# Performance work log

Measured on AMD Instinct MI355X. Metric: run time of the kernel, lower is better.

The kernel has to match this reference:

```python
import jax, jax.numpy as jnp
import numpy as np

B, C, H, W = 8, 512, 64, 64
WS, NH = 8, 16
HD = C // NH
SCALE = float(HD) ** -0.5
L = WS * WS  # tokens per window
BN_EPS = 1e-5


def _rel_index():
    # Swin relative position index, (L, L) int table into (2*WS-1)^2 bias rows
    ch = np.arange(WS)
    coords = np.stack(np.meshgrid(ch, ch, indexing='ij'))  # (2, WS, WS)
    cf = coords.reshape(2, -1)
    rel = cf[:, :, None] - cf[:, None, :]
    rel = rel.transpose(1, 2, 0).copy()
    rel[:, :, 0] += WS - 1
    rel[:, :, 1] += WS - 1
    rel[:, :, 0] *= 2 * WS - 1
    return jnp.asarray(rel.sum(-1))

REL_IDX = _rel_index()


def conv2d(x, w, pad=0, groups=1):
    return jax.lax.conv_general_dilated(
        x, w, (1, 1), [(pad, pad), (pad, pad)],
        feature_group_count=groups,
        dimension_numbers=('NCHW', 'OIHW', 'NCHW'))


def bn(x, g, b):
    # eval-mode BatchNorm with running_mean=0, running_var=1 (fresh init)
    inv = 1.0 / np.sqrt(1.0 + BN_EPS)
    return g[None, :, None, None] * (x * inv) + b[None, :, None, None]


def avgpool(x, kh, kw, ph, pw):
    # torch AvgPool2d: zero padding, count_include_pad=True
    s = jax.lax.reduce_window(x, 0.0, jax.lax.add, (1, 1, kh, kw), (1, 1, 1, 1),
                              ((0, 0), (0, 0), (ph, ph), (pw, pw)))
    return s / (kh * kw)


def setup_inputs() -> dict:
    key = jax.random.key(0)
    ks = jax.random.split(key, 8)
    r = lambda k, s: jax.random.normal(k, s, dtype=jnp.float32) * 0.02
    return {
        'x': jax.random.normal(ks[0], (B, C, H, W), dtype=jnp.float32),
        'w_lc1': r(ks[1], (C, C, 1, 1)),
        'g1': jnp.ones((C,), jnp.float32), 'b1': jnp.zeros((C,), jnp.float32),
        'w_lc2': r(ks[2], (C, C, 3, 3)),
        'g2': jnp.ones((C,), jnp.float32), 'b2': jnp.zeros((C,), jnp.float32),
        'w_qkv': r(ks[3], (3 * C, C, 1, 1)),
        'rel_table': r(ks[4], ((2 * WS - 1) * (2 * WS - 1), NH)),
        'w_dw': r(ks[5], (C, 1, WS, WS)),
        'g3': jnp.ones((C,), jnp.float32), 'b3': jnp.zeros((C,), jnp.float32),
        'w_pw': r(ks[6], (C, C, 1, 1)),
    }


def reference(x, w_lc1, g1, b1, w_lc2, g2, b2, w_qkv, rel_table, w_dw, g3, b3, w_pw):
    # local branch: 1x1 conv+BN  +  3x3 conv+BN
    local = bn(conv2d(x, w_lc1), g1, b1) + bn(conv2d(x, w_lc2, pad=1), g2, b2)

    # H, W divisible by WS -> pad() is a no-op; Hp, Wp = H, W
    hh, ww = H // WS, W // WS
    qkv = conv2d(x, w_qkv)  # (B, 3C, H, W)
    # 'b (qkv h d) (hh ws1) (ww ws2) -> qkv (b hh ww) h (ws1 ws2) d'
    qkv = qkv.reshape(B, 3, NH, HD, hh, WS, ww, WS)
    qkv = qkv.transpose(1, 0, 4, 6, 2, 5, 7, 3).reshape(3, B * hh * ww, NH, L, HD)
    q, k, v = qkv[0], qkv[1], qkv[2]

    dots = jnp.einsum('bhid,bhjd->bhij', q, k) * SCALE  # (Bw, NH, L, L)
    bias = rel_table[REL_IDX]                            # (L, L, NH)
    dots = dots + bias.transpose(2, 0, 1)[None]
    attn = jax.nn.softmax(dots, axis=-1)
    out = jnp.einsum('bhij,bhjd->bhid', attn, v)         # (Bw, NH, L, HD)

    # '(b hh ww) h (ws1 ws2) d -> b (h d) (hh ws1) (ww ws2)'
    out = out.reshape(B, hh, ww, NH, WS, WS, HD)
    out = out.transpose(0, 3, 6, 1, 4, 2, 5).reshape(B, C, H, W)

    ax = avgpool(jnp.pad(out, ((0, 0), (0, 0), (0, 1), (0, 0)), mode='reflect'),
                 WS, 1, WS // 2 - 1, 0)
    ay = avgpool(jnp.pad(out, ((0, 0), (0, 0), (0, 0), (0, 1)), mode='reflect'),
                 1, WS, 0, WS // 2 - 1)
    out = ax + ay + local

    # pad_out + SeparableConvBN(kernel=WS): depthwise conv -> BN -> 1x1 conv
    out = jnp.pad(out, ((0, 0), (0, 0), (0, 1), (0, 1)), mode='reflect')
    out = conv2d(out, w_dw, pad=(WS - 1) // 2, groups=C)
    out = bn(out, g3, b3)
    out = conv2d(out, w_pw)
    return out[:, :, :H, :W]
```

## Files before the change

### kernel.cpp

```cpp
#include <hip/hip_runtime.h>

#define INVBN 0.9999950000374997f
#define ATT_SCALE 0.17677669529663687f

typedef short bf16x8 __attribute__((ext_vector_type(8)));
typedef float f32x4  __attribute__((ext_vector_type(4)));
typedef unsigned short us8v __attribute__((ext_vector_type(8)));

#define AS1C(p) ((const __attribute__((address_space(1))) void*)(p))
#define AS3(p)  ((__attribute__((address_space(3))) void*)(p))

__device__ __forceinline__ float bf2f(unsigned short u) {
    return __uint_as_float(((unsigned)u) << 16);
}
__device__ __forceinline__ unsigned short f2bf(float f) {
    unsigned u = __float_as_uint(f);
    u += 0x7FFFu + ((u >> 16) & 1u);
    return (unsigned short)(u >> 16);
}

__global__ __launch_bounds__(256)
void repack_kernel(const float* __restrict__ W2, const float* __restrict__ W1,
                   const float* __restrict__ Wq, const float* __restrict__ Wp,
                   const float* __restrict__ g1, const float* __restrict__ g2,
                   const float* __restrict__ b1, const float* __restrict__ b2,
                   const float* __restrict__ RT,
                   unsigned short* __restrict__ Wt, unsigned short* __restrict__ WqO,
                   unsigned short* __restrict__ WpO, float* __restrict__ bsum,
                   float* __restrict__ biasM)
{
    int i = blockIdx.x * 256 + threadIdx.x;
    if (i < 512) bsum[i] = b1[i] + b2[i];
    if (i < 786432) WqO[i] = f2bf(Wq[i]);
    if (i < 262144) WpO[i] = f2bf(Wp[i]);
    if (i < 16384) {
        int h = i >> 10, rem = i & 1023;
        int frag = rem >> 6, lane = rem & 63;
        int fi = frag >> 2, fj = frag & 3;
        int q  = 16 * fj + (lane & 15);
        int kb = 16 * fi + ((lane >> 4) << 2);
        int yi = q >> 3, xi = q & 7;
        float4 o;
        float* op = (float*)&o;
#pragma unroll
        for (int r = 0; r < 4; ++r) {
            int j = kb + r;
            int ridx = (yi - (j >> 3) + 7) * 15 + (xi - (j & 7) + 7);
            op[r] = RT[ridx * 16 + h];
        }
        *(float4*)&biasM[(size_t)i * 4] = o;
    }
    if (i >= 2359296) return;
    int tap = i / 262144;
    int rem = i - tap * 262144;
    int m   = rem >> 9;
    float v = g2[m] * INVBN * W2[(size_t)rem * 9 + tap];
    if (tap == 4) v = fmaf(g1[m] * INVBN, W1[rem], v);
    Wt[i] = f2bf(v);
}

__global__ __launch_bounds__(256)
void pad_transpose_kernel(const float* __restrict__ X, unsigned short* __restrict__ XT)
{
    int ph = blockIdx.x;
    int b  = blockIdx.y;
    int t  = threadIdx.x;
    unsigned short* rowbase = XT + ((size_t)b * 4356 + (size_t)ph * 66) * 512;
    uint4 z = make_uint4(0, 0, 0, 0);
    if (ph == 0 || ph == 65) {
        uint4* p4 = (uint4*)rowbase;
        for (int i = t; i < 4224; i += 256) p4[i] = z;
        return;
    }
    if (t < 64)       ((uint4*)rowbase)[t] = z;
    else if (t < 128) ((uint4*)(rowbase + 65 * 512))[t - 64] = z;

    int h = ph - 1;
    __shared__ float tile[64][65];
    const float* xb = X + (size_t)b * 512 * 4096 + h * 64;
    for (int cc = 0; cc < 8; ++cc) {
        int c0 = cc * 64;
        __syncthreads();
#pragma unroll
        for (int i = 0; i < 4; ++i) {
            int cl = i * 16 + (t >> 4);
            int w0 = (t & 15) * 4;
            *(float4*)&tile[cl][w0] =
                *(const float4*)&xb[(size_t)(c0 + cl) * 4096 + w0];
        }
        __syncthreads();
#pragma unroll
        for (int it = 0; it < 2; ++it) {
            int wl = it * 32 + (t >> 3);
            int cs = (t & 7) * 8;
            us8v v;
#pragma unroll
            for (int e = 0; e < 8; ++e) v[e] = f2bf(tile[cs + e][wl]);
            *(us8v*)&rowbase[(size_t)(1 + wl) * 512 + c0 + cs] = v;
        }
    }
}

template<int NTAPS>
__global__ __launch_bounds__(256, 2)
void mfma_gemm256(const unsigned short* __restrict__ A,
                  const unsigned short* __restrict__ Bw,
                  const float* __restrict__ bias,
                  unsigned short* __restrict__ Out, int M, int MB)
{
    __shared__ __align__(16) unsigned short ldsbuf[36864];

    const int t    = threadIdx.x;
    const int wid  = t >> 6, lane = t & 63;
    const int wr   = wid >> 1, wc = wid & 1;
    const int lrow = lane & 15, lk = lane >> 4;

    const int nwg = gridDim.x;
    const int id  = blockIdx.x;
    const int cid = (id & 7) * (nwg >> 3) + (id >> 3);
    const int by  = cid % MB;
    const int rst = cid / MB;
    const int bx  = rst & 15;
    const int bz  = rst >> 4;

    const int n0 = bx * 256;
    const int m0 = by * 128;
    const unsigned short* Ab = A + (size_t)bz * (4356 * 512);
    unsigned short* Ob = Out + (size_t)bz * ((size_t)M * 4096);

    const int rsub = t >> 2, ch = t & 3;
    const int chs  = ch ^ ((rsub >> 1) & 3);
    const unsigned short* asrc[4];
    const unsigned short* bsrc[2];
#pragma unroll
    for (int i = 0; i < 4; ++i) {
        int p = n0 + i * 64 + rsub;
        int h = p >> 6, w = p & 63;
        asrc[i] = Ab + (size_t)((h + 1) * 66 + (w + 1)) * 512 + chs * 8;
    }
#pragma unroll
    for (int j = 0; j < 2; ++j)
        bsrc[j] = Bw + (size_t)(m0 + j * 64 + rsub) * 512 + chs * 8;

    f32x4 acc[8][4] = {};
    const int ck0 = (lk ^ ((lrow >> 1) & 3)) * 8;

    auto aScal = [&](int tt) -> int {
        if (NTAPS == 1) return tt * 32;
        int tap = tt >> 4;
        return (tap / 3 - 1) * (66 * 512) + (tap % 3 - 1) * 512 + (tt & 15) * 32;
    };
    auto bScal = [&](int tt) -> int {
        if (NTAPS == 1) return tt * 32;
        return (tt >> 4) * (M * 512) + (tt & 15) * 32;
    };
    auto STAGE = [&](int bufk, int tt) {
        unsigned short* dst = ldsbuf + bufk * 12288;
        int ao = aScal(tt), bo = bScal(tt);
#pragma unroll
        for (int i = 0; i < 4; ++i)
            __builtin_amdgcn_global_load_lds(
                AS1C(asrc[i] + ao), AS3(dst + (i * 64 + rsub) * 32 + ch * 8), 16, 0, 0);
#pragma unroll
        for (int j = 0; j < 2; ++j)
            __builtin_amdgcn_global_load_lds(
                AS1C(bsrc[j] + bo), AS3(dst + 8192 + (j * 64 + rsub) * 32 + ch * 8), 16, 0, 0);
    };
    auto COMPUTE = [&](int bufk) {
        const unsigned short* Ak = ldsbuf + bufk * 12288;
        const unsigned short* Bk = Ak + 8192;
        bf16x8 af[8], bf[4];
#pragma unroll
        for (int f = 0; f < 8; ++f)
            af[f] = *(const bf16x8*)&Ak[(wr * 128 + f * 16 + lrow) * 32 + ck0];
#pragma unroll
        for (int g = 0; g < 4; ++g)
            bf[g] = *(const bf16x8*)&Bk[(wc * 64 + g * 16 + lrow) * 32 + ck0];
        __builtin_amdgcn_s_setprio(1);
#pragma unroll
        for (int f = 0; f < 8; ++f)
#pragma unroll
            for (int g = 0; g < 4; ++g)
                acc[f][g] = __builtin_amdgcn_mfma_f32_16x16x32_bf16(
                    af[f], bf[g], acc[f][g], 0, 0, 0);
        __builtin_amdgcn_s_setprio(0);
    };

    constexpr int NT = NTAPS * 16;

    STAGE(0, 0);
    STAGE(1, 1);
    int cur = 0, nxt = 1, prv = 2;
#pragma unroll 1
    for (int tt = 0; tt < NT; ++tt) {
        if (tt + 2 < NT) {
            STAGE(prv, tt + 2);
            asm volatile("s_waitcnt vmcnt(6)" ::: "memory");
        } else if (tt + 1 < NT) {
            asm volatile("s_waitcnt vmcnt(6)" ::: "memory");
        } else {
            asm volatile("s_waitcnt vmcnt(0)" ::: "memory");
        }
        __builtin_amdgcn_s_barrier();
        COMPUTE(cur);
        __builtin_amdgcn_s_barrier();
        int tmp = prv; prv = cur; cur = nxt; nxt = tmp;
    }

#pragma unroll
    for (int g = 0; g < 4; ++g) {
        int m = m0 + wc * 64 + g * 16 + lrow;
        float bv = bias ? bias[m] : 0.f;
        size_t mrow = (size_t)m * 4096;
#pragma unroll
        for (int f = 0; f < 8; ++f) {
            int nb = n0 + wr * 128 + f * 16 + lk * 4;
            f32x4 a4 = acc[f][g];
            ushort4 o;
            o.x = f2bf(a4[0] + bv);
            o.y = f2bf(a4[1] + bv);
            o.z = f2bf(a4[2] + bv);
            o.w = f2bf(a4[3] + bv);
            *(ushort4*)&Ob[mrow + nb] = o;
        }
    }
}

__global__ __launch_bounds__(256)
void mfma_gemm_f32out(const unsigned short* __restrict__ A,
                      const unsigned short* __restrict__ Bw,
                      float* __restrict__ Out, int M)
{
    __shared__ short As[128 * 64];
    __shared__ short Bs[128 * 64];

    const int t  = threadIdx.x;
    const int n0 = blockIdx.x * 128;
    const int m0 = blockIdx.y * 128;
    const int b  = blockIdx.z;
    const unsigned short* Ab = A + (size_t)b * (4096 * 512);
    float* Ob = Out + (size_t)b * ((size_t)M * 4096);

    const int trow = t >> 3;
    const int csrc = (t & 7) ^ (trow & 7);
    const unsigned short* aSrc[4];
    const unsigned short* bSrc[4];
#pragma unroll
    for (int i = 0; i < 4; ++i) {
        int r = i * 32 + trow;
        aSrc[i] = Ab + ((size_t)(n0 + r) * 512 + csrc * 8);
        bSrc[i] = Bw + ((size_t)(m0 + r) * 512 + csrc * 8);
    }
    short* aDst = As + (t & 192) * 8;
    short* bDst = Bs + (t & 192) * 8;

    const int lane = t & 63;
    const int wv = t >> 6, wr = wv >> 1, wc = wv & 1;
    const int lrow = lane & 15, lk = lane >> 4;
    int aOff[4][2], bOff[4][2];
#pragma unroll
    for (int f = 0; f < 4; ++f)
#pragma unroll
        for (int kk = 0; kk < 2; ++kk) {
            int ra = wr * 64 + f * 16 + lrow;
            aOff[f][kk] = ra * 64 + ((kk * 4 + lk) ^ (ra & 7)) * 8;
            int rb = wc * 64 + f * 16 + lrow;
            bOff[f][kk] = rb * 64 + ((kk * 4 + lk) ^ (rb & 7)) * 8;
        }

    f32x4 acc[4][4] = {};

#pragma unroll 1
    for (int ks = 0; ks < 8; ++ks) {
        const int k0 = ks * 64;
        __syncthreads();
#pragma unroll
        for (int i = 0; i < 4; ++i) {
            __builtin_amdgcn_global_load_lds(
                AS1C(aSrc[i] + k0), AS3(aDst + i * 2048), 16, 0, 0);
            __builtin_amdgcn_global_load_lds(
                AS1C(bSrc[i] + k0), AS3(bDst + i * 2048), 16, 0, 0);
        }
        __syncthreads();
        bf16x8 av[4][2], bv[4][2];
#pragma unroll
        for (int f = 0; f < 4; ++f) {
            av[f][0] = *(const bf16x8*)&As[aOff[f][0]];
            av[f][1] = *(const bf16x8*)&As[aOff[f][1]];
            bv[f][0] = *(const bf16x8*)&Bs[bOff[f][0]];
            bv[f][1] = *(const bf16x8*)&Bs[bOff[f][1]];
        }
#pragma unroll
        for (int kk = 0; kk < 2; ++kk)
#pragma unroll
            for (int fn = 0; fn < 4; ++fn)
#pragma unroll
                for (int fm = 0; fm < 4; ++fm)
                    acc[fn][fm] = __builtin_amdgcn_mfma_f32_16x16x32_bf16(
                        av[fn][kk], bv[fm][kk], acc[fn][fm], 0, 0, 0);
    }

#pragma unroll
    for (int fm = 0; fm < 4; ++fm) {
        int m = m0 + wc * 64 + fm * 16 + lrow;
        size_t mrow = (size_t)m * 4096;
#pragma unroll
        for (int fn = 0; fn < 4; ++fn) {
            int nb = n0 + wr * 64 + fn * 16 + lk * 4;
            f32x4 a4 = acc[fn][fm];
            *(float4*)&Ob[mrow + nb] = make_float4(a4[0], a4[1], a4[2], a4[3]);
        }
    }
}

__global__ __launch_bounds__(256)
void attn_mfma_kernel(const unsigned short* __restrict__ QKV,
                      const float* __restrict__ biasM,
                      unsigned short* __restrict__ OutB)
{
    __shared__ short smem[4 * 9216];
    int t = threadIdx.x;
    int wv = t >> 6, lane = t & 63;
    int wing = blockIdx.x >> 2;
    int head = (blockIdx.x & 3) * 4 + wv;
    int b    = blockIdx.y;
    int hhi = wing >> 3, wwi = wing & 7;
    int sp0 = hhi * 512 + wwi * 8;
    int ch0 = head * 32;
    const unsigned short* Qg = QKV + (size_t)b * 1536 * 4096;

    short* Qtm = smem + wv * 9216;
    short* Ktm = Qtm + 2304;
    short* Pq  = Qtm + 4608;

    {
        int d  = lane & 31;
        int rb = lane >> 5;
#pragma unroll
        for (int i = 0; i < 4; ++i) {
            int r = rb + 2 * i;
            us8v q8 = *(const us8v*)&Qg[(size_t)(ch0 + d) * 4096 + sp0 + r * 64];
            us8v k8 = *(const us8v*)&Qg[(size_t)(512 + ch0 + d) * 4096 + sp0 + r * 64];
#pragma unroll
            for (int e = 0; e < 8; ++e) {
                Qtm[(r * 8 + e) * 36 + d] = (short)q8[e];
                Ktm[(r * 8 + e) * 36 + d] = (short)k8[e];
            }
        }
    }

    int lrow = lane & 15, lk = lane >> 4;

    bf16x8 kf[4], qf[4];
#pragma unroll
    for (int f = 0; f < 4; ++f) {
        kf[f] = *(const bf16x8*)&Ktm[(lrow + 16 * f) * 36 + lk * 8];
        qf[f] = *(const bf16x8*)&Qtm[(lrow + 16 * f) * 36 + lk * 8];
    }
    f32x4 s[4][4] = {};
#pragma unroll
    for (int fi = 0; fi < 4; ++fi)
#pragma unroll
        for (int fj = 0; fj < 4; ++fj)
            s[fi][fj] = __builtin_amdgcn_mfma_f32_16x16x32_bf16(
                kf[fi], qf[fj], s[fi][fj], 0, 0, 0);

    const float* bM = biasM + (size_t)head * 4096;
    float rs[4];
#pragma unroll
    for (int fj = 0; fj < 4; ++fj) {
        float v[4][4];
#pragma unroll
        for (int fi = 0; fi < 4; ++fi) {
            float4 bv = *(const float4*)&bM[((fi * 4 + fj) * 64 + lane) * 4];
            const float* bvp = (const float*)&bv;
#pragma unroll
            for (int r = 0; r < 4; ++r)
                v[fi][r] = fmaf(s[fi][fj][r], ATT_SCALE, bvp[r]);
        }
        float m = -1e30f;
#pragma unroll
        for (int fi = 0; fi < 4; ++fi)
#pragma unroll
            for (int r = 0; r < 4; ++r) m = fmaxf(m, v[fi][r]);
        m = fmaxf(m, __shfl_xor(m, 16));
        m = fmaxf(m, __shfl_xor(m, 32));
        float ev[4][4];
        float sum = 0.f;
#pragma unroll
        for (int fi = 0; fi < 4; ++fi)
#pragma unroll
            for (int r = 0; r < 4; ++r) {
                ev[fi][r] = __expf(v[fi][r] - m);
                sum += ev[fi][r];
            }
        sum += __shfl_xor(sum, 16);
        sum += __shfl_xor(sum, 32);
        rs[fj] = 1.f / sum;
#pragma unroll
        for (int fi = 0; fi < 4; ++fi) {
            unsigned p0 = (unsigned)f2bf(ev[fi][0]) | ((unsigned)f2bf(ev[fi][1]) << 16);
            unsigned p1 = (unsigned)f2bf(ev[fi][2]) | ((unsigned)f2bf(ev[fi][3]) << 16);
            *(uint2*)&Pq[(lrow + 16 * fj) * 72 + 16 * fi + lk * 4] = make_uint2(p0, p1);
        }
    }

    f32x4 o[2][4] = {};
#pragma unroll
    for (int ks = 0; ks < 2; ++ks) {
        bf16x8 vf[2], pf[4];
#pragma unroll
        for (int fid = 0; fid < 2; ++fid)
            vf[fid] = *(const bf16x8*)&Qg[(size_t)(1024 + ch0 + 16 * fid + lrow) * 4096
                                          + sp0 + (lk + 4 * ks) * 64];
#pragma unroll
        for (int fjq = 0; fjq < 4; ++fjq)
            pf[fjq] = *(const bf16x8*)&Pq[(lrow + 16 * fjq) * 72 + ks * 32 + lk * 8];
#pragma unroll
        for (int fid = 0; fid < 2; ++fid)
#pragma unroll
            for (int fjq = 0; fjq < 4; ++fjq)
                o[fid][fjq] = __builtin_amdgcn_mfma_f32_16x16x32_bf16(
                    vf[fid], pf[fjq], o[fid][fjq], 0, 0, 0);
    }

#pragma unroll
    for (int fjq = 0; fjq < 4; ++fjq) {
        int q = lrow + 16 * fjq;
        float rr = rs[fjq];
#pragma unroll
        for (int fid = 0; fid < 2; ++fid) {
            int dch = 16 * fid + lk * 4;
#pragma unroll
            for (int r = 0; r < 4; ++r)
                Pq[(dch + r) * 72 + q] = (short)f2bf(o[fid][fjq][r] * rr);
        }
    }
    unsigned short* Out = OutB + (size_t)b * 512 * 4096;
#pragma unroll
    for (int j = 0; j < 4; ++j) {
        int dch  = lane & 31;
        int tokc = (lane >> 5) + 2 * j;
        us8v vv = *(const us8v*)&Pq[dch * 72 + tokc * 8];
        *(us8v*)&Out[(size_t)(ch0 + dch) * 4096 + sp0 + tokc * 64] = vv;
    }
}

__global__ __launch_bounds__(256)
void pooldw_kernel(const unsigned short* __restrict__ A, const unsigned short* __restrict__ L,
                   const float* __restrict__ Wd,
                   const float* __restrict__ g3, const float* __restrict__ b3,
                   unsigned short* __restrict__ U)
{
    int bc = blockIdx.x;
    int c  = bc & 511;
    __shared__ float pad[72][72];
    int t = threadIdx.x;
    float* pf = &pad[0][0];
#pragma unroll
    for (int i = 0; i < 21; ++i) {
        int e = i * 256 + t;
        if (e < 5184) pf[e] = 0.f;
    }
    __syncthreads();

    const unsigned short* ap = A + (size_t)bc * 4096;
#pragma unroll
    for (int i = 0; i < 4; ++i) {
        int idx = i * 256 + t;
        int y = idx >> 4, x4 = (idx & 15) * 4;
        ushort4 a4 = ((const ushort4*)ap)[idx];
        *(float4*)&pad[3 + y][4 + x4] =
            make_float4(bf2f(a4.x), bf2f(a4.y), bf2f(a4.z), bf2f(a4.w));
    }
    if (t < 64)       pad[67][4 + t] = bf2f(ap[62 * 64 + t]);
    else if (t < 128) { int y = t - 64; pad[3 + y][68] = bf2f(ap[y * 64 + 62]); }
    else if (t == 128) pad[67][68] = bf2f(ap[62 * 64 + 62]);
    __syncthreads();

    const unsigned short* lp = L + (size_t)bc * 4096;
    int u  = t & 7, rr = t >> 3;
    int w0 = u * 8;
    float res[2][8];
#pragma unroll
    for (int g = 0; g < 2; ++g) {
        int h = g * 32 + rr;
        float4 sxlo = make_float4(0.f, 0.f, 0.f, 0.f);
        float4 sxhi = make_float4(0.f, 0.f, 0.f, 0.f);
#pragma unroll
        for (int i = 0; i < 8; ++i) {
            float4 a = *(const float4*)&pad[h + i][4 + w0];
            float4 bq = *(const float4*)&pad[h + i][8 + w0];
            sxlo.x += a.x; sxlo.y += a.y; sxlo.z += a.z; sxlo.w += a.w;
            sxhi.x += bq.x; sxhi.y += bq.y; sxhi.z += bq.z; sxhi.w += bq.w;
        }
        float sx[8] = {sxlo.x, sxlo.y, sxlo.z, sxlo.w, sxhi.x, sxhi.y, sxhi.z, sxhi.w};
        float win[16];
        *(float4*)&win[0]  = *(const float4*)&pad[3 + h][w0];
        *(float4*)&win[4]  = *(const float4*)&pad[3 + h][w0 + 4];
        *(float4*)&win[8]  = *(const float4*)&pad[3 + h][w0 + 8];
        *(float4*)&win[12] = *(const float4*)&pad[3 + h][w0 + 12];
        us8v l8 = *(const us8v*)&lp[h * 64 + w0];
#pragma unroll
        for (int p = 0; p < 8; ++p) {
            float sy = 0.f;
#pragma unroll
            for (int i = 1; i <= 8; ++i) sy += win[p + i];
            res[g][p] = fmaf(0.125f, sx[p] + sy, bf2f((unsigned short)l8[p]));
        }
    }
    __syncthreads();

#pragma unroll
    for (int g = 0; g < 2; ++g) {
        int h = g * 32 + rr;
        *(float4*)&pad[3 + h][4 + w0] = make_float4(res[g][0], res[g][1], res[g][2], res[g][3]);
        *(float4*)&pad[3 + h][8 + w0] = make_float4(res[g][4], res[g][5], res[g][6], res[g][7]);
    }
    __syncthreads();
    if (t < 64)       pad[67][4 + t] = pad[65][4 + t];
    else if (t < 128) { int y = t - 64; pad[3 + y][68] = pad[3 + y][66]; }
    else if (t == 128) pad[67][68] = pad[65][66];
    __syncthreads();

    const float* wdp = Wd + c * 64;
    float gc  = g3[c] * INVBN;
    float bcv = b3[c];
#pragma unroll
    for (int g = 0; g < 2; ++g) {
        int h = g * 32 + rr;
        float acc2[8];
#pragma unroll
        for (int p = 0; p < 8; ++p) acc2[p] = 0.f;
#pragma unroll
        for (int i = 0; i < 8; ++i) {
            float win[16];
            *(float4*)&win[0]  = *(const float4*)&pad[h + i][w0];
            *(float4*)&win[4]  = *(const float4*)&pad[h + i][w0 + 4];
            *(float4*)&win[8]  = *(const float4*)&pad[h + i][w0 + 8];
            *(float4*)&win[12] = *(const float4*)&pad[h + i][w0 + 12];
#pragma unroll
            for (int j = 0; j < 8; ++j) {
                float wv = wdp[i * 8 + j];
#pragma unroll
                for (int p = 0; p < 8; ++p)
                    acc2[p] = fmaf(wv, win[p + 1 + j], acc2[p]);
            }
        }
        us8v o8;
#pragma unroll
        for (int p = 0; p < 8; ++p) o8[p] = (short)f2bf(gc * acc2[p] + bcv);
        *(us8v*)&U[(size_t)bc * 4096 + h * 64 + w0] = o8;
    }
}

__global__ __launch_bounds__(256)
void transpose_cp_kernel(const unsigned short* __restrict__ U, unsigned short* __restrict__ Ut)
{
    int pt = blockIdx.x;
    int b  = blockIdx.y;
    const unsigned short* Ub = U + (size_t)b * 512 * 4096;
    unsigned short* Utb = Ut + (size_t)b * 4096 * 512;
    __shared__ unsigned short tile[64][72];
    int t = threadIdx.x;
    int p0 = pt * 64;

    for (int cc = 0; cc < 8; ++cc) {
        int c0 = cc * 64;
        __syncthreads();
        {
            int cl = t >> 2, px = (t & 3) * 16;
            const unsigned short* src = &Ub[(size_t)(c0 + cl) * 4096 + p0 + px];
            *(us8v*)&tile[cl][px]     = *(const us8v*)src;
            *(us8v*)&tile[cl][px + 8] = *(const us8v*)(src + 8);
        }
        __syncthreads();
        {
            int pl = t >> 2, cx = (t & 3) * 16;
            us8v o0, o1;
#pragma unroll
            for (int e = 0; e < 8; ++e) {
                o0[e] = tile[cx + e][pl];
                o1[e] = tile[cx + 8 + e][pl];
            }
            unsigned short* dst = &Utb[(size_t)(p0 + pl) * 512 + c0 + cx];
            *(us8v*)dst       = o0;
            *(us8v*)(dst + 8) = o1;
        }
    }
}

extern "C" void kernel_launch(void* const* d_in, const int* in_sizes, int n_in,
                              void* d_out, int out_size, void* d_ws, size_t ws_size,
                              hipStream_t stream)
{
    (void)in_sizes; (void)n_in; (void)out_size;
    const float* x     = (const float*)d_in[0];
    const float* w_lc1 = (const float*)d_in[1];
    const float* g1    = (const float*)d_in[2];
    const float* b1    = (const float*)d_in[3];
    const float* w_lc2 = (const float*)d_in[4];
    const float* g2    = (const float*)d_in[5];
    const float* b2    = (const float*)d_in[6];
    const float* w_qkv = (const float*)d_in[7];
    const float* rt    = (const float*)d_in[8];
    const float* w_dw  = (const float*)d_in[9];
    const float* g3    = (const float*)d_in[10];
    const float* b3    = (const float*)d_in[11];
    const float* w_pw  = (const float*)d_in[12];
    float* out = (float*)d_out;

    unsigned short* S        = (unsigned short*)d_ws;
    unsigned short* local_us = S;
    unsigned short* xt_us    = S + 16777216;
    unsigned short* attnO    = xt_us;
    unsigned short* u_us     = xt_us;
    unsigned short* wt3_us   = S + 34619392;
    unsigned short* wq_us    = S + 36978688;
    unsigned short* wpw_us   = S + 37765120;
    float*          bsum     = (float*)(S + 38027264);
    float*          biasM    = (float*)(S + 38028288);
    unsigned short* qkv_us   = S + 38552576;
    unsigned short* ut_us    = local_us;

    const bool full = ws_size >= (size_t)(38552576 + 50331648) * 2;

    repack_kernel<<<dim3(9216), 256, 0, stream>>>(w_lc2, w_lc1, w_qkv, w_pw,
                                                  g1, g2, b1, b2, rt,
                                                  wt3_us, wq_us, wpw_us, bsum, biasM);
    pad_transpose_kernel<<<dim3(66, 8), 256, 0, stream>>>(x, xt_us);
    mfma_gemm256<9><<<dim3(512), 256, 0, stream>>>(
        xt_us, wt3_us, bsum, local_us, 512, 4);

    if (full) {
        mfma_gemm256<1><<<dim3(1536), 256, 0, stream>>>(
            xt_us, wq_us, nullptr, qkv_us, 1536, 12);
        attn_mfma_kernel<<<dim3(256, 8), 256, 0, stream>>>(qkv_us, biasM, attnO);
    } else {
        for (int b = 0; b < 8; ++b) {
            mfma_gemm256<1><<<dim3(192), 256, 0, stream>>>(
                xt_us + (size_t)b * 4356 * 512, wq_us, nullptr, qkv_us, 1536, 12);
            attn_mfma_kernel<<<dim3(256, 1), 256, 0, stream>>>(
                qkv_us, biasM, attnO + (size_t)b * 2097152);
        }
    }

    pooldw_kernel<<<dim3(4096), 256, 0, stream>>>(attnO, local_us, w_dw, g3, b3, u_us);
    transpose_cp_kernel<<<dim3(64, 8), 256, 0, stream>>>(u_us, ut_us);
    mfma_gemm_f32out<<<dim3(32, 4, 8), 256, 0, stream>>>(
        ut_us, wpw_us, out, 512);
}
```

Measured before the change: 481.1 us.

## Use 8-wave 256x256 GEMM tile with 4-stage LDS pipeline and unify GEMMs

The bf16 GEMM kernel moves from 4 waves with a 256x128 tile to 8 waves with a 256x256 tile. Four waves load A and four load B into a 4-buffer LDS ring, with a single waitcnt plus barrier per k-step instead of two barriers. The separate f32-output pointwise GEMM is replaced by a templated instance of the same kernel, and the workgroup-id swizzle gives way to a plain 3D grid. This is meant to raise data reuse per tile and deepen prefetch, at the cost of 128KB of LDS, higher register pressure, and fewer workgroups in flight.

```diff
diff --git a/kernel.cpp b/kernel.cpp
--- a/kernel.cpp
+++ b/kernel.cpp
@@ -9,6 +9,10 @@
 
 #define AS1C(p) ((const __attribute__((address_space(1))) void*)(p))
 #define AS3(p)  ((__attribute__((address_space(3))) void*)(p))
+
+#define VMCNT_BARRIER(Nstr) do {                                   \
+    asm volatile("s_waitcnt vmcnt(" Nstr ")" ::: "memory");        \
+    __builtin_amdgcn_s_barrier(); } while (0)
 
 __device__ __forceinline__ float bf2f(unsigned short u) {
     return __uint_as_float(((unsigned)u) << 16);
@@ -101,48 +105,48 @@
     }
 }
 
-template<int NTAPS>
-__global__ __launch_bounds__(256, 2)
+template<int NTAPS, bool PAD, typename OT>
+__global__ __launch_bounds__(512, 2)
 void mfma_gemm256(const unsigned short* __restrict__ A,
                   const unsigned short* __restrict__ Bw,
                   const float* __restrict__ bias,
-                  unsigned short* __restrict__ Out, int M, int MB)
-{
-    __shared__ __align__(16) unsigned short ldsbuf[36864];
+                  OT* __restrict__ Out, int M)
+{
+    __shared__ __align__(16) unsigned short ldsbuf[65536];
 
     const int t    = threadIdx.x;
     const int wid  = t >> 6, lane = t & 63;
-    const int wr   = wid >> 1, wc = wid & 1;
+    const int wr   = wid >> 2, wc = wid & 3;
     const int lrow = lane & 15, lk = lane >> 4;
-
-    const int nwg = gridDim.x;
-    const int id  = blockIdx.x;
-    const int cid = (id & 7) * (nwg >> 3) + (id >> 3);
-    const int by  = cid % MB;
-    const int rst = cid / MB;
-    const int bx  = rst & 15;
-    const int bz  = rst >> 4;
-
-    const int n0 = bx * 256;
-    const int m0 = by * 128;
-    const unsigned short* Ab = A + (size_t)bz * (4356 * 512);
-    unsigned short* Ob = Out + (size_t)bz * ((size_t)M * 4096);
-
-    const int rsub = t >> 2, ch = t & 3;
-    const int chs  = ch ^ ((rsub >> 1) & 3);
-    const unsigned short* asrc[4];
-    const unsigned short* bsrc[2];
-#pragma unroll
-    for (int i = 0; i < 4; ++i) {
-        int p = n0 + i * 64 + rsub;
-        int h = p >> 6, w = p & 63;
-        asrc[i] = Ab + (size_t)((h + 1) * 66 + (w + 1)) * 512 + chs * 8;
-    }
-#pragma unroll
-    for (int j = 0; j < 2; ++j)
-        bsrc[j] = Bw + (size_t)(m0 + j * 64 + rsub) * 512 + chs * 8;
+    const int n0 = blockIdx.x * 256;
+    const int m0 = blockIdx.y * 256;
+    const int b  = blockIdx.z;
+    const unsigned short* Ab = A + (size_t)b * (PAD ? 4356 * 512 : 4096 * 512);
+    OT* Ob = Out + (size_t)b * ((size_t)M * 4096);
+
+    const unsigned short* src[4];
+    {
+        int rsub = lane >> 2, ch = lane & 3;
+        int chs  = ch ^ ((rsub >> 1) & 3);
+#pragma unroll
+        for (int i = 0; i < 4; ++i) {
+            if (wid < 4) {
+                int p = n0 + (wid * 4 + i) * 16 + rsub;
+                if (PAD) {
+                    int h = p >> 6, w = p & 63;
+                    src[i] = Ab + (size_t)((h + 1) * 66 + (w + 1)) * 512 + chs * 8;
+                } else {
+                    src[i] = Ab + (size_t)p * 512 + chs * 8;
+                }
+            } else {
+                int m = m0 + ((wid - 4) * 4 + i) * 16 + rsub;
+                src[i] = Bw + (size_t)m * 512 + chs * 8;
+            }
+        }
+    }
 
     f32x4 acc[8][4] = {};
+
     const int ck0 = (lk ^ ((lrow >> 1) & 3)) * 8;
 
     auto aScal = [&](int tt) -> int {
@@ -154,58 +158,52 @@
         if (NTAPS == 1) return tt * 32;
         return (tt >> 4) * (M * 512) + (tt & 15) * 32;
     };
-    auto STAGE = [&](int bufk, int tt) {
-        unsigned short* dst = ldsbuf + bufk * 12288;
-        int ao = aScal(tt), bo = bScal(tt);
+    auto STAGE = [&](int bufk, int aoff, int boff) {
+        int off = (wid < 4) ? aoff : boff;
 #pragma unroll
         for (int i = 0; i < 4; ++i)
             __builtin_amdgcn_global_load_lds(
-                AS1C(asrc[i] + ao), AS3(dst + (i * 64 + rsub) * 32 + ch * 8), 16, 0, 0);
-#pragma unroll
-        for (int j = 0; j < 2; ++j)
-            __builtin_amdgcn_global_load_lds(
-                AS1C(bsrc[j] + bo), AS3(dst + 8192 + (j * 64 + rsub) * 32 + ch * 8), 16, 0, 0);
+                AS1C(src[i] + off),
+                AS3(&ldsbuf[bufk * 16384 + (wid * 4 + i) * 512]), 16, 0, 0);
     };
     auto COMPUTE = [&](int bufk) {
-        const unsigned short* Ak = ldsbuf + bufk * 12288;
-        const unsigned short* Bk = Ak + 8192;
-        bf16x8 af[8], bf[4];
+        const unsigned short* Ak = &ldsbuf[bufk * 16384];
+        const unsigned short* Bk = &ldsbuf[bufk * 16384 + 8192];
+        bf16x8 af[8], bfr[4];
 #pragma unroll
         for (int f = 0; f < 8; ++f)
             af[f] = *(const bf16x8*)&Ak[(wr * 128 + f * 16 + lrow) * 32 + ck0];
 #pragma unroll
         for (int g = 0; g < 4; ++g)
-            bf[g] = *(const bf16x8*)&Bk[(wc * 64 + g * 16 + lrow) * 32 + ck0];
+            bfr[g] = *(const bf16x8*)&Bk[(wc * 64 + g * 16 + lrow) * 32 + ck0];
         __builtin_amdgcn_s_setprio(1);
 #pragma unroll
         for (int f = 0; f < 8; ++f)
 #pragma unroll
             for (int g = 0; g < 4; ++g)
                 acc[f][g] = __builtin_amdgcn_mfma_f32_16x16x32_bf16(
-                    af[f], bf[g], acc[f][g], 0, 0, 0);
+                    af[f], bfr[g], acc[f][g], 0, 0, 0);
         __builtin_amdgcn_s_setprio(0);
     };
 
     constexpr int NT = NTAPS * 16;
 
-    STAGE(0, 0);
-    STAGE(1, 1);
-    int cur = 0, nxt = 1, prv = 2;
+    STAGE(0, aScal(0), bScal(0));
+    STAGE(1, aScal(1), bScal(1));
+    STAGE(2, aScal(2), bScal(2));
+    VMCNT_BARRIER("8");
+
 #pragma unroll 1
-    for (int tt = 0; tt < NT; ++tt) {
-        if (tt + 2 < NT) {
-            STAGE(prv, tt + 2);
-            asm volatile("s_waitcnt vmcnt(6)" ::: "memory");
-        } else if (tt + 1 < NT) {
-            asm volatile("s_waitcnt vmcnt(6)" ::: "memory");
-        } else {
-            asm volatile("s_waitcnt vmcnt(0)" ::: "memory");
-        }
-        __builtin_amdgcn_s_barrier();
-        COMPUTE(cur);
-        __builtin_amdgcn_s_barrier();
-        int tmp = prv; prv = cur; cur = nxt; nxt = tmp;
-    }
+    for (int tb = 0; tb < NT - 4; tb += 4) {
+        STAGE(3, aScal(tb + 3), bScal(tb + 3)); COMPUTE(0); VMCNT_BARRIER("8");
+        STAGE(0, aScal(tb + 4), bScal(tb + 4)); COMPUTE(1); VMCNT_BARRIER("8");
+        STAGE(1, aScal(tb + 5), bScal(tb + 5)); COMPUTE(2); VMCNT_BARRIER("8");
+        STAGE(2, aScal(tb + 6), bScal(tb + 6)); COMPUTE(3); VMCNT_BARRIER("8");
+    }
+    STAGE(3, aScal(NT - 1), bScal(NT - 1)); COMPUTE(0); VMCNT_BARRIER("8");
+    COMPUTE(1); VMCNT_BARRIER("4");
+    COMPUTE(2); VMCNT_BARRIER("0");
+    COMPUTE(3);
 
 #pragma unroll
     for (int g = 0; g < 4; ++g) {
@@ -216,99 +214,17 @@
         for (int f = 0; f < 8; ++f) {
             int nb = n0 + wr * 128 + f * 16 + lk * 4;
             f32x4 a4 = acc[f][g];
-            ushort4 o;
-            o.x = f2bf(a4[0] + bv);
-            o.y = f2bf(a4[1] + bv);
-            o.z = f2bf(a4[2] + bv);
-            o.w = f2bf(a4[3] + bv);
-            *(ushort4*)&Ob[mrow + nb] = o;
-        }
-    }
-}
-
-__global__ __launch_bounds__(256)
-void mfma_gemm_f32out(const unsigned short* __restrict__ A,
-                      const unsigned short* __restrict__ Bw,
-                      float* __restrict__ Out, int M)
-{
-    __shared__ short As[128 * 64];
-    __shared__ short Bs[128 * 64];
-
-    const int t  = threadIdx.x;
-    const int n0 = blockIdx.x * 128;
-    const int m0 = blockIdx.y * 128;
-    const int b  = blockIdx.z;
-    const unsigned short* Ab = A + (size_t)b * (4096 * 512);
-    float* Ob = Out + (size_t)b * ((size_t)M * 4096);
-
-    const int trow = t >> 3;
-    const int csrc = (t & 7) ^ (trow & 7);
-    const unsigned short* aSrc[4];
-    const unsigned short* bSrc[4];
-#pragma unroll
-    for (int i = 0; i < 4; ++i) {
-        int r = i * 32 + trow;
-        aSrc[i] = Ab + ((size_t)(n0 + r) * 512 + csrc * 8);
-        bSrc[i] = Bw + ((size_t)(m0 + r) * 512 + csrc * 8);
-    }
-    short* aDst = As + (t & 192) * 8;
-    short* bDst = Bs + (t & 192) * 8;
-
-    const int lane = t & 63;
-    const int wv = t >> 6, wr = wv >> 1, wc = wv & 1;
-    const int lrow = lane & 15, lk = lane >> 4;
-    int aOff[4][2], bOff[4][2];
-#pragma unroll
-    for (int f = 0; f < 4; ++f)
-#pragma unroll
-        for (int kk = 0; kk < 2; ++kk) {
-            int ra = wr * 64 + f * 16 + lrow;
-            aOff[f][kk] = ra * 64 + ((kk * 4 + lk) ^ (ra & 7)) * 8;
-            int rb = wc * 64 + f * 16 + lrow;
-            bOff[f][kk] = rb * 64 + ((kk * 4 + lk) ^ (rb & 7)) * 8;
-        }
-
-    f32x4 acc[4][4] = {};
-
-#pragma unroll 1
-    for (int ks = 0; ks < 8; ++ks) {
-        const int k0 = ks * 64;
-        __syncthreads();
-#pragma unroll
-        for (int i = 0; i < 4; ++i) {
-            __builtin_amdgcn_global_load_lds(
-                AS1C(aSrc[i] + k0), AS3(aDst + i * 2048), 16, 0, 0);
-            __builtin_amdgcn_global_load_lds(
-                AS1C(bSrc[i] + k0), AS3(bDst + i * 2048), 16, 0, 0);
-        }
-        __syncthreads();
-        bf16x8 av[4][2], bv[4][2];
-#pragma unroll
-        for (int f = 0; f < 4; ++f) {
-            av[f][0] = *(const bf16x8*)&As[aOff[f][0]];
-            av[f][1] = *(const bf16x8*)&As[aOff[f][1]];
-            bv[f][0] = *(const bf16x8*)&Bs[bOff[f][0]];
-            bv[f][1] = *(const bf16x8*)&Bs[bOff[f][1]];
-        }
-#pragma unroll
-        for (int kk = 0; kk < 2; ++kk)
-#pragma unroll
-            for (int fn = 0; fn < 4; ++fn)
-#pragma unroll
-                for (int fm = 0; fm < 4; ++fm)
-                    acc[fn][fm] = __builtin_amdgcn_mfma_f32_16x16x32_bf16(
-                        av[fn][kk], bv[fm][kk], acc[fn][fm], 0, 0, 0);
-    }
-
-#pragma unroll
-    for (int fm = 0; fm < 4; ++fm) {
-        int m = m0 + wc * 64 + fm * 16 + lrow;
-        size_t mrow = (size_t)m * 4096;
-#pragma unroll
-        for (int fn = 0; fn < 4; ++fn) {
-            int nb = n0 + wr * 64 + fn * 16 + lk * 4;
-            f32x4 a4 = acc[fn][fm];
-            *(float4*)&Ob[mrow + nb] = make_float4(a4[0], a4[1], a4[2], a4[3]);
+            if constexpr (sizeof(OT) == 2) {
+                ushort4 o;
+                o.x = f2bf(a4[0] + bv);
+                o.y = f2bf(a4[1] + bv);
+                o.z = f2bf(a4[2] + bv);
+                o.w = f2bf(a4[3] + bv);
+                *(ushort4*)&Ob[mrow + nb] = o;
+            } else {
+                *(float4*)&Ob[mrow + nb] =
+                    make_float4(a4[0] + bv, a4[1] + bv, a4[2] + bv, a4[3] + bv);
+            }
         }
     }
 }
@@ -629,17 +545,17 @@
                                                   g1, g2, b1, b2, rt,
                                                   wt3_us, wq_us, wpw_us, bsum, biasM);
     pad_transpose_kernel<<<dim3(66, 8), 256, 0, stream>>>(x, xt_us);
-    mfma_gemm256<9><<<dim3(512), 256, 0, stream>>>(
-        xt_us, wt3_us, bsum, local_us, 512, 4);
+    mfma_gemm256<9, true, unsigned short><<<dim3(16, 2, 8), 512, 0, stream>>>(
+        xt_us, wt3_us, bsum, local_us, 512);
 
     if (full) {
-        mfma_gemm256<1><<<dim3(1536), 256, 0, stream>>>(
-            xt_us, wq_us, nullptr, qkv_us, 1536, 12);
+        mfma_gemm256<1, true, unsigned short><<<dim3(16, 6, 8), 512, 0, stream>>>(
+            xt_us, wq_us, nullptr, qkv_us, 1536);
         attn_mfma_kernel<<<dim3(256, 8), 256, 0, stream>>>(qkv_us, biasM, attnO);
     } else {
         for (int b = 0; b < 8; ++b) {
-            mfma_gemm256<1><<<dim3(192), 256, 0, stream>>>(
-                xt_us + (size_t)b * 4356 * 512, wq_us, nullptr, qkv_us, 1536, 12);
+            mfma_gemm256<1, true, unsigned short><<<dim3(16, 6, 1), 512, 0, stream>>>(
+                xt_us + (size_t)b * 4356 * 512, wq_us, nullptr, qkv_us, 1536);
             attn_mfma_kernel<<<dim3(256, 1), 256, 0, stream>>>(
                 qkv_us, biasM, attnO + (size_t)b * 2097152);
         }
@@ -647,6 +563,6 @@
 
     pooldw_kernel<<<dim3(4096), 256, 0, stream>>>(attnO, local_us, w_dw, g3, b3, u_us);
     transpose_cp_kernel<<<dim3(64, 8), 256, 0, stream>>>(u_us, ut_us);
-    mfma_gemm_f32out<<<dim3(32, 4, 8), 256, 0, stream>>>(
-        ut_us, wpw_us, out, 512);
-}
+    mfma_gemm256<1, false, float><<<dim3(16, 2, 8), 512, 0, stream>>>(
+        ut_us, wpw_us, nullptr, out, 512);
+}
```

Result: faster. 466.3 us (median of 3 runs) (-3.1%).
